# Optimization experiments

Hardware: AMD Instinct MI355X
Metric: run time of the kernel (lower is better)

Reference implementation:

```python
import jax, jax.numpy as jnp
import numpy as np

SIGNAL_LEN = 2048
N_WAVELETS = 32
TWO_PI = 2.0 * np.pi


def _encoder(x, W1, b1, W2, b2, W3, b3, W4, b4):
    B = x.shape[0]
    h = x.reshape(B, -1)                      # (B, 4096)
    h = jax.nn.relu(h @ W1.T + b1)            # (B, 1024)
    h = jax.nn.relu(h @ W2.T + b2)            # (B, 512)
    h = jax.nn.relu(h @ W3.T + b3)            # (B, 256)
    return h @ W4.T + b4                      # (B, n_wavelets*5)


def _synthesize(params):
    # params: (B, N_WAVELETS, 5)
    A = params[..., 0]                                    # (B, N)
    t0 = jax.nn.sigmoid(params[..., 1]) * SIGNAL_LEN      # (B, N)
    f = jax.nn.sigmoid(params[..., 2]) * 0.5              # (B, N)
    sigma = jax.nn.sigmoid(params[..., 3]) * 200.0 + 2.0  # (B, N)
    phi = params[..., 4]                                  # (B, N)

    t = jnp.arange(SIGNAL_LEN, dtype=params.dtype)        # (T,)
    dt = t[None, None, :] - t0[..., None]                 # (B, N, T)
    g = (A[..., None]
         * jnp.exp(-(dt * dt) / (2.0 * sigma[..., None] ** 2))
         * jnp.cos(TWO_PI * f[..., None] * dt + phi[..., None]))  # (B, N, T)
    sig = jnp.sum(g, axis=1)                              # (B, T)
    # both channels receive the identical wavelet sum (as in the torch code)
    return jnp.stack([sig, sig], axis=1)                  # (B, 2, T)


def setup_inputs() -> dict:
    key = jax.random.key(0)
    ks = jax.random.split(key, 9)
    B = 4096
    def w(k, shape, fan_in):
        return jax.random.normal(k, shape, dtype=jnp.float32) / np.sqrt(fan_in)
    return {
        "x": jax.random.normal(ks[0], (B, 2, SIGNAL_LEN), dtype=jnp.float32),
        "W1": w(ks[1], (1024, 4096), 4096), "b1": jnp.zeros((1024,), jnp.float32),
        "W2": w(ks[2], (512, 1024), 1024),  "b2": jnp.zeros((512,), jnp.float32),
        "W3": w(ks[3], (256, 512), 512),    "b3": jnp.zeros((256,), jnp.float32),
        "W4": w(ks[4], (N_WAVELETS * 5, 256), 256), "b4": jnp.zeros((N_WAVELETS * 5,), jnp.float32),
    }


def reference(x, W1, b1, W2, b2, W3, b3, W4, b4):
    B = x.shape[0]
    params = _encoder(x, W1, b1, W2, b2, W3, b3, W4, b4).reshape(B, N_WAVELETS, 5)
    return _synthesize(params)  # (B, 2, SIGNAL_LEN)
```

## Files before the change

### kernel.cpp

```cpp
#include <hip/hip_runtime.h>


#define SIGNAL_LEN 2048
#define NWAV 32

typedef _Float16 f16x8 __attribute__((ext_vector_type(8)));
typedef _Float16 f16x4 __attribute__((ext_vector_type(4)));
typedef float    f32x4 __attribute__((ext_vector_type(4)));

__device__ __forceinline__ void load16_lds(const _Float16* g, _Float16* l) {
  __builtin_amdgcn_global_load_lds((const __attribute__((address_space(1))) void*)g,
                                   (__attribute__((address_space(3))) void*)l,
                                   16, 0, 0);
}

struct HL { _Float16 h, l; };
__device__ __forceinline__ HL split_one(float a) {
  HL r;
  r.h = (_Float16)a;
  r.l = (_Float16)((a - (float)r.h) * 4096.0f);
  return r;
}

__global__ void split_x(const float4* __restrict__ src, f16x4* __restrict__ dh,
                        f16x4* __restrict__ dl) {
  int i = blockIdx.x * 256 + threadIdx.x;
  float4 v = src[i];
  float a[4] = {v.x, v.y, v.z, v.w};
  f16x4 h, l;
#pragma unroll
  for (int j = 0; j < 4; j++) {
    HL r = split_one(a[j]);
    h[j] = r.h;
    l[j] = r.l;
  }
  dh[i] = h;
  dl[i] = l;
}

__global__ void split_weights(const float* __restrict__ W1, const float* __restrict__ W2,
                              const float* __restrict__ W3, const float* __restrict__ W4,
                              const float* __restrict__ b4,
                              f16x4* __restrict__ W1h, f16x4* __restrict__ W1l,
                              f16x4* __restrict__ W2h, f16x4* __restrict__ W2l,
                              f16x4* __restrict__ W3h, f16x4* __restrict__ W3l,
                              f16x4* __restrict__ W4h, f16x4* __restrict__ W4l,
                              float* __restrict__ b4p) {
  const int blk = blockIdx.x;
  const int tid = threadIdx.x;
  if (blk < 4736) {
    const float4* src;
    f16x4 *dh, *dl;
    int i;
    if (blk < 4096) {
      src = (const float4*)W1; dh = W1h; dl = W1l; i = blk * 256 + tid;
    } else if (blk < 4608) {
      src = (const float4*)W2; dh = W2h; dl = W2l; i = (blk - 4096) * 256 + tid;
    } else {
      src = (const float4*)W3; dh = W3h; dl = W3l; i = (blk - 4608) * 256 + tid;
    }
    float4 v = src[i];
    float a[4] = {v.x * 256.0f, v.y * 256.0f, v.z * 256.0f, v.w * 256.0f};
    f16x4 h, l;
#pragma unroll
    for (int j = 0; j < 4; j++) {
      HL r = split_one(a[j]);
      h[j] = r.h;
      l[j] = r.l;
    }
    dh[i] = h;
    dl[i] = l;
  } else if (blk < 4800) {
    int i = (blk - 4736) * 256 + tid;
    int i4 = i << 2;
    int row = i4 >> 8;
    f16x4 h, l;
#pragma unroll
    for (int j = 0; j < 4; j++) {
      float a = (row < 160) ? W4[i4 + j] * 256.0f : 0.0f;
      HL r = split_one(a);
      h[j] = r.h;
      l[j] = r.l;
    }
    W4h[i] = h;
    W4l[i] = l;
  } else {
    b4p[tid] = (tid < 160) ? b4[tid] : 0.0f;
  }
}

template <int TM, int TN, int N, int K, bool RELU, bool SPLIT_OUT>
__global__ void __launch_bounds__(256, 2)
gemm_db(const _Float16* __restrict__ Ah, const _Float16* __restrict__ Al,
        const _Float16* __restrict__ Bh, const _Float16* __restrict__ Bl,
        const float* __restrict__ bias,
        _Float16* __restrict__ Ch, _Float16* __restrict__ Cl,
        float* __restrict__ Cf) {
  constexpr int AM = TM / 32;
  constexpr int BN = TN / 32;
  constexpr int AU = TM / 8;
  constexpr int TU = (TM + TN) / 8;
  constexpr int UPW = TU / 4;
  constexpr int NK = K / 32;

  __shared__ __align__(16) _Float16 s[2][(TM + TN) * 64];

  const int tid = threadIdx.x;
  const int lane = tid & 63;
  const int w = tid >> 6;
  const int wm = w >> 1, wn = w & 1;
  const int m0 = blockIdx.y * TM;
  const int n0 = blockIdx.x * TN;

  const int srow = lane >> 2;
  const int sk8 = (((lane & 3) - (lane >> 3)) & 3) * 8;

  const _Float16* gb[UPW];
  int lo[UPW];
#pragma unroll
  for (int i = 0; i < UPW; ++i) {
    const int u = w * UPW + i;
    if (u < AU) {
      const int g = u >> 1, hl = u & 1;
      gb[i] = (hl ? Al : Ah) + (size_t)(m0 + g * 16 + srow) * K + sk8;
    } else {
      const int ub = u - AU;
      const int g = ub >> 1, hl = ub & 1;
      gb[i] = (hl ? Bl : Bh) + (size_t)(n0 + g * 16 + srow) * K + sk8;
    }
    lo[i] = u * 512;
  }

  const int fr = lane & 15;
  const int fq = lane >> 4;
  const int fslot8 = (4 * fr + ((fq + (fr >> 1)) & 3)) * 8;

  f32x4 acc1[AM][BN], acc2[AM][BN];
#pragma unroll
  for (int i = 0; i < AM; i++)
#pragma unroll
    for (int j = 0; j < BN; j++) {
      acc1[i][j] = 0.0f;
      acc2[i][j] = 0.0f;
    }

#pragma unroll
  for (int i = 0; i < UPW; ++i) load16_lds(gb[i], &s[0][lo[i]]);

  for (int kt = 0; kt < NK; ++kt) {
    const int cur = kt & 1;
    __syncthreads();

    if (kt + 1 < NK) {
      const int kofs = (kt + 1) * 32;
#pragma unroll
      for (int i = 0; i < UPW; ++i) load16_lds(gb[i] + kofs, &s[cur ^ 1][lo[i]]);
    }

    f16x8 fAh[AM], fAl[AM], fBh[BN], fBl[BN];
#pragma unroll
    for (int im = 0; im < AM; ++im) {
      const int g = wm * AM + im;
      fAh[im] = *(const f16x8*)(&s[cur][(g * 2 + 0) * 512 + fslot8]);
      fAl[im] = *(const f16x8*)(&s[cur][(g * 2 + 1) * 512 + fslot8]);
    }
#pragma unroll
    for (int in = 0; in < BN; ++in) {
      const int g = wn * BN + in;
      fBh[in] = *(const f16x8*)(&s[cur][TM * 64 + (g * 2 + 0) * 512 + fslot8]);
      fBl[in] = *(const f16x8*)(&s[cur][TM * 64 + (g * 2 + 1) * 512 + fslot8]);
    }
#pragma unroll
    for (int im = 0; im < AM; ++im) {
#pragma unroll
      for (int in = 0; in < BN; ++in) {
        acc1[im][in] = __builtin_amdgcn_mfma_f32_16x16x32_f16(fAh[im], fBh[in], acc1[im][in], 0, 0, 0);
        acc2[im][in] = __builtin_amdgcn_mfma_f32_16x16x32_f16(fAh[im], fBl[in], acc2[im][in], 0, 0, 0);
        acc2[im][in] = __builtin_amdgcn_mfma_f32_16x16x32_f16(fAl[im], fBh[in], acc2[im][in], 0, 0, 0);
      }
    }
  }

  const int quad = lane >> 4;
#pragma unroll
  for (int in = 0; in < BN; ++in) {
    const int n = n0 + wn * (TN / 2) + in * 16 + fr;
    const float bv = bias[n];
#pragma unroll
    for (int im = 0; im < AM; ++im) {
#pragma unroll
      for (int r = 0; r < 4; ++r) {
        const int m = m0 + wm * (TM / 2) + im * 16 + quad * 4 + r;
        float c = (acc1[im][in][r] + acc2[im][in][r] * (1.0f / 4096.0f)) * (1.0f / 256.0f) + bv;
        if (RELU) c = fmaxf(c, 0.0f);
        const size_t off = (size_t)m * N + n;
        if (SPLIT_OUT) {
          HL rr = split_one(c);
          Ch[off] = rr.h;
          Cl[off] = rr.l;
        } else {
          Cf[off] = c;
        }
      }
    }
  }
}

__global__ void __launch_bounds__(256)
synth(const float* __restrict__ P, float* __restrict__ out) {
  __shared__ float sA[NWAV], sT0[NWAV], sF[NWAV], sC[NWAV], sPh[NWAV], sSg[NWAV];
  const int b = blockIdx.x;
  const int tid = threadIdx.x;
  if (tid < NWAV) {
    const float* q = P + (size_t)b * 256 + tid * 5;
    const float L2E = 1.44269504088896340736f;
    float A = q[0], p1 = q[1], p2 = q[2], p3 = q[3], p4 = q[4];
    float s1 = 1.0f / (1.0f + exp2f(-p1 * L2E));
    float s2 = 1.0f / (1.0f + exp2f(-p2 * L2E));
    float s3 = 1.0f / (1.0f + exp2f(-p3 * L2E));
    float sg = s3 * 200.0f + 2.0f;
    sA[tid] = A;
    sT0[tid] = s1 * 2048.0f;
    sF[tid] = s2 * 0.5f;
    sC[tid] = -L2E / (2.0f * sg * sg);
    sPh[tid] = p4 * 0.15915494309189535f;
    sSg[tid] = sg;
  }
  __syncthreads();

  const float t0f = (float)(tid * 8);
  const int wlo = (tid & ~63) * 8;
  float acc[8];
#pragma unroll
  for (int i = 0; i < 8; i++) acc[i] = 0.0f;

  for (int wv = 0; wv < NWAV; wv++) {
    const float t0 = sT0[wv], sg = sSg[wv];
    if (t0 + 5.0f * sg < (float)wlo || t0 - 5.0f * sg > (float)(wlo + 511)) continue;
    const float A = sA[wv], fr = sF[wv], cn = sC[wv], ph = sPh[wv];
#pragma unroll
    for (int i = 0; i < 8; i++) {
      float dt = (t0f + (float)i) - t0;
      float e = exp2f(dt * dt * cn);
      float r = fr * dt + ph;
      r -= floorf(r);
      float cs = __builtin_amdgcn_cosf(r);
      acc[i] += A * e * cs;
    }
  }

  float* o = out + (size_t)b * (2 * SIGNAL_LEN) + tid * 8;
  float4 v0 = make_float4(acc[0], acc[1], acc[2], acc[3]);
  float4 v1 = make_float4(acc[4], acc[5], acc[6], acc[7]);
  *(float4*)(o) = v0;
  *(float4*)(o + 4) = v1;
  *(float4*)(o + SIGNAL_LEN) = v0;
  *(float4*)(o + SIGNAL_LEN + 4) = v1;
}

extern "C" void kernel_launch(void* const* d_in, const int* in_sizes, int n_in,
                              void* d_out, int out_size, void* d_ws, size_t ws_size,
                              hipStream_t stream) {
  (void)in_sizes; (void)n_in; (void)out_size; (void)ws_size;
  const float* X  = (const float*)d_in[0];
  const float* W1 = (const float*)d_in[1];
  const float* b1 = (const float*)d_in[2];
  const float* W2 = (const float*)d_in[3];
  const float* b2 = (const float*)d_in[4];
  const float* W3 = (const float*)d_in[5];
  const float* b3 = (const float*)d_in[6];
  const float* W4 = (const float*)d_in[7];
  const float* b4 = (const float*)d_in[8];
  float* out = (float*)d_out;

  char* p = (char*)d_ws;
  auto take = [&](size_t bytes) -> char* {
    char* r = p;
    p += (bytes + 255) & ~(size_t)255;
    return r;
  };
  _Float16* Xh  = (_Float16*)take((size_t)4096 * 4096 * 2);
  _Float16* Xl  = (_Float16*)take((size_t)4096 * 4096 * 2);
  _Float16* W1h = (_Float16*)take((size_t)1024 * 4096 * 2);
  _Float16* W1l = (_Float16*)take((size_t)1024 * 4096 * 2);
  _Float16* H1h = (_Float16*)take((size_t)4096 * 1024 * 2);
  _Float16* H1l = (_Float16*)take((size_t)4096 * 1024 * 2);
  _Float16* W2h = (_Float16*)take((size_t)512 * 1024 * 2);
  _Float16* W2l = (_Float16*)take((size_t)512 * 1024 * 2);
  _Float16* H2h = (_Float16*)take((size_t)4096 * 512 * 2);
  _Float16* H2l = (_Float16*)take((size_t)4096 * 512 * 2);
  _Float16* W3h = (_Float16*)take((size_t)256 * 512 * 2);
  _Float16* W3l = (_Float16*)take((size_t)256 * 512 * 2);
  _Float16* H3h = (_Float16*)take((size_t)4096 * 256 * 2);
  _Float16* H3l = (_Float16*)take((size_t)4096 * 256 * 2);
  _Float16* W4h = (_Float16*)take((size_t)256 * 256 * 2);
  _Float16* W4l = (_Float16*)take((size_t)256 * 256 * 2);
  float*    b4p = (float*)take(256 * 4);
  float*    Pp  = (float*)take((size_t)4096 * 256 * 4);

  split_x<<<16384, 256, 0, stream>>>((const float4*)X, (f16x4*)Xh, (f16x4*)Xl);
  split_weights<<<4801, 256, 0, stream>>>(W1, W2, W3, W4, b4,
                                          (f16x4*)W1h, (f16x4*)W1l, (f16x4*)W2h, (f16x4*)W2l,
                                          (f16x4*)W3h, (f16x4*)W3l, (f16x4*)W4h, (f16x4*)W4l, b4p);

  gemm_db<128, 128, 1024, 4096, true, true><<<dim3(8, 32), 256, 0, stream>>>(
      Xh, Xl, W1h, W1l, b1, H1h, H1l, nullptr);
  gemm_db<64, 128, 512, 1024, true, true><<<dim3(4, 64), 256, 0, stream>>>(
      H1h, H1l, W2h, W2l, b2, H2h, H2l, nullptr);
  gemm_db<64, 64, 256, 512, true, true><<<dim3(4, 64), 256, 0, stream>>>(
      H2h, H2l, W3h, W3l, b3, H3h, H3l, nullptr);
  gemm_db<64, 64, 256, 256, false, false><<<dim3(4, 64), 256, 0, stream>>>(
      H3h, H3l, W4h, W4l, b4p, nullptr, nullptr, Pp);

  synth<<<4096, 256, 0, stream>>>(Pp, out);
}
```

Measured before the change: 403.8 us.

## Split first GEMM along K into two partial passes with fp32 fixup kernel

New measurement: 406.3 us. Within noise of the previous version (+0.6%).

```diff
diff --git a/kernel.cpp b/kernel.cpp
--- a/kernel.cpp
+++ b/kernel.cpp
@@ -89,7 +89,7 @@
   }
 }
 
-template <int TM, int TN, int N, int K, bool RELU, bool SPLIT_OUT>
+template <int TM, int TN, int N, int KSTR, int KBLK, bool RELU, bool SPLIT_OUT, bool PARTIAL>
 __global__ void __launch_bounds__(256, 2)
 gemm_db(const _Float16* __restrict__ Ah, const _Float16* __restrict__ Al,
         const _Float16* __restrict__ Bh, const _Float16* __restrict__ Bl,
@@ -101,7 +101,7 @@
   constexpr int AU = TM / 8;
   constexpr int TU = (TM + TN) / 8;
   constexpr int UPW = TU / 4;
-  constexpr int NK = K / 32;
+  constexpr int NK = KBLK / 32;
 
   __shared__ __align__(16) _Float16 s[2][(TM + TN) * 64];
 
@@ -111,6 +111,7 @@
   const int wm = w >> 1, wn = w & 1;
   const int m0 = blockIdx.y * TM;
   const int n0 = blockIdx.x * TN;
+  const size_t kb = (size_t)blockIdx.z * KBLK;
 
   const int srow = lane >> 2;
   const int sk8 = (((lane & 3) - (lane >> 3)) & 3) * 8;
@@ -122,11 +123,11 @@
     const int u = w * UPW + i;
     if (u < AU) {
       const int g = u >> 1, hl = u & 1;
-      gb[i] = (hl ? Al : Ah) + (size_t)(m0 + g * 16 + srow) * K + sk8;
+      gb[i] = (hl ? Al : Ah) + (size_t)(m0 + g * 16 + srow) * KSTR + kb + sk8;
     } else {
       const int ub = u - AU;
       const int g = ub >> 1, hl = ub & 1;
-      gb[i] = (hl ? Bl : Bh) + (size_t)(n0 + g * 16 + srow) * K + sk8;
+      gb[i] = (hl ? Bl : Bh) + (size_t)(n0 + g * 16 + srow) * KSTR + kb + sk8;
     }
     lo[i] = u * 512;
   }
@@ -182,28 +183,59 @@
   }
 
   const int quad = lane >> 4;
+  float* Cfz = Cf;
+  if (PARTIAL) Cfz = Cf + (size_t)blockIdx.z * gridDim.y * TM * N;
 #pragma unroll
   for (int in = 0; in < BN; ++in) {
     const int n = n0 + wn * (TN / 2) + in * 16 + fr;
-    const float bv = bias[n];
+    float bv = 0.0f;
+    if (!PARTIAL) bv = bias[n];
 #pragma unroll
     for (int im = 0; im < AM; ++im) {
 #pragma unroll
       for (int r = 0; r < 4; ++r) {
         const int m = m0 + wm * (TM / 2) + im * 16 + quad * 4 + r;
-        float c = (acc1[im][in][r] + acc2[im][in][r] * (1.0f / 4096.0f)) * (1.0f / 256.0f) + bv;
-        if (RELU) c = fmaxf(c, 0.0f);
         const size_t off = (size_t)m * N + n;
-        if (SPLIT_OUT) {
-          HL rr = split_one(c);
-          Ch[off] = rr.h;
-          Cl[off] = rr.l;
+        if (PARTIAL) {
+          Cfz[off] = acc1[im][in][r] + acc2[im][in][r] * (1.0f / 4096.0f);
         } else {
-          Cf[off] = c;
+          float c = (acc1[im][in][r] + acc2[im][in][r] * (1.0f / 4096.0f)) * (1.0f / 256.0f) + bv;
+          if (RELU) c = fmaxf(c, 0.0f);
+          if (SPLIT_OUT) {
+            HL rr = split_one(c);
+            Ch[off] = rr.h;
+            Cl[off] = rr.l;
+          } else {
+            Cf[off] = c;
+          }
         }
       }
     }
   }
+}
+
+__global__ void fixup_g1(const float4* __restrict__ P0, const float4* __restrict__ P1,
+                         const float* __restrict__ b1,
+                         f16x4* __restrict__ Hh, f16x4* __restrict__ Hl) {
+  const int i = blockIdx.x * 256 + threadIdx.x;
+  const int n4 = (i << 2) & 1023;
+  float4 p0 = P0[i];
+  float4 p1 = P1[i];
+  float4 bv = *(const float4*)(b1 + n4);
+  float a[4] = {(p0.x + p1.x) * (1.0f / 256.0f) + bv.x,
+                (p0.y + p1.y) * (1.0f / 256.0f) + bv.y,
+                (p0.z + p1.z) * (1.0f / 256.0f) + bv.z,
+                (p0.w + p1.w) * (1.0f / 256.0f) + bv.w};
+  f16x4 h, l;
+#pragma unroll
+  for (int j = 0; j < 4; j++) {
+    float c = fmaxf(a[j], 0.0f);
+    HL r = split_one(c);
+    h[j] = r.h;
+    l[j] = r.l;
+  }
+  Hh[i] = h;
+  Hl[i] = l;
 }
 
 __global__ void __launch_bounds__(256)
@@ -297,19 +329,23 @@
   _Float16* W4l = (_Float16*)take((size_t)256 * 256 * 2);
   float*    b4p = (float*)take(256 * 4);
   float*    Pp  = (float*)take((size_t)4096 * 256 * 4);
+  float*    Pk  = (float*)take((size_t)2 * 4096 * 1024 * 4);
 
   split_x<<<16384, 256, 0, stream>>>((const float4*)X, (f16x4*)Xh, (f16x4*)Xl);
   split_weights<<<4801, 256, 0, stream>>>(W1, W2, W3, W4, b4,
                                           (f16x4*)W1h, (f16x4*)W1l, (f16x4*)W2h, (f16x4*)W2l,
                                           (f16x4*)W3h, (f16x4*)W3l, (f16x4*)W4h, (f16x4*)W4l, b4p);
 
-  gemm_db<128, 128, 1024, 4096, true, true><<<dim3(8, 32), 256, 0, stream>>>(
-      Xh, Xl, W1h, W1l, b1, H1h, H1l, nullptr);
-  gemm_db<64, 128, 512, 1024, true, true><<<dim3(4, 64), 256, 0, stream>>>(
+  gemm_db<128, 128, 1024, 4096, 2048, false, false, true><<<dim3(8, 32, 2), 256, 0, stream>>>(
+      Xh, Xl, W1h, W1l, nullptr, nullptr, nullptr, Pk);
+  fixup_g1<<<4096, 256, 0, stream>>>((const float4*)Pk, (const float4*)(Pk + (size_t)4096 * 1024),
+                                     b1, (f16x4*)H1h, (f16x4*)H1l);
+
+  gemm_db<64, 64, 512, 1024, 1024, true, true, false><<<dim3(8, 64, 1), 256, 0, stream>>>(
       H1h, H1l, W2h, W2l, b2, H2h, H2l, nullptr);
-  gemm_db<64, 64, 256, 512, true, true><<<dim3(4, 64), 256, 0, stream>>>(
+  gemm_db<64, 64, 256, 512, 512, true, true, false><<<dim3(4, 64, 1), 256, 0, stream>>>(
       H2h, H2l, W3h, W3l, b3, H3h, H3l, nullptr);
-  gemm_db<64, 64, 256, 256, false, false><<<dim3(4, 64), 256, 0, stream>>>(
+  gemm_db<64, 64, 256, 256, 256, false, false, false><<<dim3(4, 64, 1), 256, 0, stream>>>(
       H3h, H3l, W4h, W4l, b4p, nullptr, nullptr, Pp);
 
   synth<<<4096, 256, 0, stream>>>(Pp, out);
```
